# Kernel tuning notes

Measured on AMD Instinct MI355X. Metric: run time of the kernel, lower is better.

## Reference

```python
import jax, jax.numpy as jnp
import numpy as np

DIM = 4096
N_HEADS = 32
N_KV_HEADS = 8
HEAD_DIM = DIM // N_HEADS  # 128
B, S = 2, 2048
LN_EPS = 1e-5


def _precompute_freqs_cis(seqlen, head_dim, theta=10000.0):
    inv = 1.0 / (theta ** (np.arange(0, head_dim, 2, dtype=np.float32) / head_dim))  # [HD/2]
    ang = np.outer(np.arange(seqlen, dtype=np.float32), inv)  # [S, HD/2]
    return jnp.asarray(np.stack([np.cos(ang), np.sin(ang)], axis=-1))  # [S, HD/2, 2]


def setup_inputs() -> dict:
    key = jax.random.key(0)
    ks = jax.random.split(key, 9)
    std = 0.02
    return {
        "x": jax.random.normal(ks[0], (B, S, DIM), dtype=jnp.float32),
        "freqs_cis": _precompute_freqs_cis(S, HEAD_DIM),
        "wq": jax.random.normal(ks[1], (N_HEADS * HEAD_DIM, DIM), dtype=jnp.float32) * std,
        "wk": jax.random.normal(ks[2], (N_KV_HEADS * HEAD_DIM, DIM), dtype=jnp.float32) * std,
        "wv": jax.random.normal(ks[3], (N_KV_HEADS * HEAD_DIM, DIM), dtype=jnp.float32) * std,
        "wo": jax.random.normal(ks[4], (DIM, N_HEADS * HEAD_DIM), dtype=jnp.float32) * std,
        "q_norm_w": jnp.ones((N_HEADS * HEAD_DIM,), dtype=jnp.float32),
        "q_norm_b": jnp.zeros((N_HEADS * HEAD_DIM,), dtype=jnp.float32),
        "k_norm_w": jnp.ones((N_KV_HEADS * HEAD_DIM,), dtype=jnp.float32),
        "k_norm_b": jnp.zeros((N_KV_HEADS * HEAD_DIM,), dtype=jnp.float32),
    }


def _layernorm(v, w, b):
    mu = jnp.mean(v, axis=-1, keepdims=True)
    var = jnp.var(v, axis=-1, keepdims=True)
    return (v - mu) * jax.lax.rsqrt(var + LN_EPS) * w + b


def _rope(t, fc):
    # t: [B, S, nh, HD]; fc: [S, HD/2, 2] = (cos, sin)
    b_, s_, nh, hd = t.shape
    tr = t.reshape(b_, s_, nh, hd // 2, 2)
    a, bb = tr[..., 0], tr[..., 1]
    cos = fc[None, :, None, :, 0]
    sin = fc[None, :, None, :, 1]
    out = jnp.stack([a * cos - bb * sin, a * sin + bb * cos], axis=-1)
    return out.reshape(t.shape)


def reference(x, freqs_cis, wq, wk, wv, wo, q_norm_w, q_norm_b, k_norm_w, k_norm_b):
    bsz, seqlen, _ = x.shape
    H, KV, HD = N_HEADS, N_KV_HEADS, HEAD_DIM
    R = H // KV  # GQA repeat factor

    xq = jnp.einsum('bsd,ed->bse', x, wq)
    xk = jnp.einsum('bsd,ed->bse', x, wk)
    xv = jnp.einsum('bsd,ed->bse', x, wv)

    xq = _layernorm(xq, q_norm_w, q_norm_b)
    xk = _layernorm(xk, k_norm_w, k_norm_b)

    xq = xq.reshape(bsz, seqlen, H, HD)
    xk = xk.reshape(bsz, seqlen, KV, HD)
    xv = xv.reshape(bsz, seqlen, KV, HD)

    xq = _rope(xq, freqs_cis)
    xk = _rope(xk, freqs_cis)

    # GQA: group q heads as (kv, rep) and broadcast k/v instead of materializing repeats
    xqg = xq.reshape(bsz, seqlen, KV, R, HD)
    scale = 1.0 / jnp.sqrt(jnp.float32(HD))
    scores = jnp.einsum('bqkrh,bskh->bkrqs', xqg, xk) * scale  # [B,KV,R,S,S]
    attn = jax.nn.softmax(scores, axis=-1)
    out = jnp.einsum('bkrqs,bskh->bqkrh', attn, xv).reshape(bsz, seqlen, H * HD)
    return jnp.einsum('bse,de->bsd', out, wo)
```

## Files before the change

kernel.cpp:

```cpp
#include <hip/hip_runtime.h>
#include <cstdint>

typedef _Float16 half4v __attribute__((ext_vector_type(4)));
typedef _Float16 half8v __attribute__((ext_vector_type(8)));
typedef __fp16   fp16x2 __attribute__((ext_vector_type(2)));
typedef float    f32x4v __attribute__((ext_vector_type(4)));

#define DIM    4096
#define SEQ    2048
#define NBATCH 2
#define NHEAD  32
#define NKVH   8
#define HDIM   128
#define MROWS  (NBATCH*SEQ)
#define QKV_N  6144
#define KOFF   4096
#define VOFF   5120

__device__ __forceinline__ void gl_lds16(const _Float16* g, _Float16* l) {
  __builtin_amdgcn_global_load_lds(
      (const __attribute__((address_space(1))) void*)g,
      (__attribute__((address_space(3))) void*)l, 16, 0, 0);
}

__global__ __launch_bounds__(256) void cvt_kernel(const float* __restrict__ in,
                                                  _Float16* __restrict__ out, int n8) {
  int stride = gridDim.x * blockDim.x;
  for (int i = blockIdx.x * blockDim.x + threadIdx.x; i < n8; i += stride) {
    const float4* p = (const float4*)(in + (size_t)i * 8);
    float4 a = p[0], b = p[1];
    half8v h;
    h[0] = (_Float16)a.x; h[1] = (_Float16)a.y; h[2] = (_Float16)a.z; h[3] = (_Float16)a.w;
    h[4] = (_Float16)b.x; h[5] = (_Float16)b.y; h[6] = (_Float16)b.z; h[7] = (_Float16)b.w;
    *(half8v*)(out + (size_t)i * 8) = h;
  }
}

template<int OUTF16>
__global__ __launch_bounds__(256, 2) void gemm_bt(const _Float16* __restrict__ A,
                                                  const _Float16* __restrict__ B,
                                                  void* __restrict__ Cp, int N, int K) {
  __shared__ __align__(16) _Float16 As[128 * 64];
  __shared__ __align__(16) _Float16 Bs[128 * 64];
  const int tid = threadIdx.x, lane = tid & 63, w = tid >> 6;
  const int g = lane >> 4, li = lane & 15;
  const int bm = blockIdx.y * 128, bn = blockIdx.x * 128;
  const int wr = (w >> 1) * 64, wc = (w & 1) * 64;
  f32x4v acc[4][4] = {};
  const int srow = lane >> 3;
  const int scol = (lane & 7) * 8;
  const _Float16* Abase = A + (size_t)bm * K + scol;
  const _Float16* Bbase = B + (size_t)bn * K + scol;
  const int nkt = K >> 6;
  for (int kt = 0; kt < nkt; ++kt) {
#pragma unroll
    for (int i = 0; i < 4; ++i) {
      const int chunk = i * 4 + w;
      const int row = chunk * 8 + srow;
      gl_lds16(Abase + (size_t)row * K + kt * 64, As + chunk * 512);
      gl_lds16(Bbase + (size_t)row * K + kt * 64, Bs + chunk * 512);
    }
    __syncthreads();
#pragma unroll
    for (int kk = 0; kk < 2; ++kk) {
      half8v af[4], bf[4];
#pragma unroll
      for (int mi = 0; mi < 4; ++mi)
        af[mi] = *(const half8v*)(As + (wr + mi * 16 + li) * 64 + kk * 32 + g * 8);
#pragma unroll
      for (int ni = 0; ni < 4; ++ni)
        bf[ni] = *(const half8v*)(Bs + (wc + ni * 16 + li) * 64 + kk * 32 + g * 8);
#pragma unroll
      for (int mi = 0; mi < 4; ++mi)
#pragma unroll
        for (int ni = 0; ni < 4; ++ni)
          acc[mi][ni] = __builtin_amdgcn_mfma_f32_16x16x32_f16(af[mi], bf[ni], acc[mi][ni], 0, 0, 0);
    }
    __syncthreads();
  }
  const int r0 = bm + wr + g * 4, c0 = bn + wc + li;
#pragma unroll
  for (int mi = 0; mi < 4; ++mi)
#pragma unroll
    for (int ni = 0; ni < 4; ++ni)
#pragma unroll
      for (int j = 0; j < 4; ++j) {
        size_t idx = (size_t)(r0 + mi * 16 + j) * N + (c0 + ni * 16);
        if (OUTF16) ((_Float16*)Cp)[idx] = (_Float16)acc[mi][ni][j];
        else        ((float*)Cp)[idx]    = acc[mi][ni][j];
      }
}

template<int E>
__global__ __launch_bounds__(256) void ln_rope(_Float16* __restrict__ t, int ldt,
                                               const float* __restrict__ gw,
                                               const float* __restrict__ gb,
                                               const float* __restrict__ fc) {
  constexpr int EPT = E / 256;
  const int row = blockIdx.x;
  const int s = row & (SEQ - 1);
  const int tid = threadIdx.x, lane = tid & 63, w = tid >> 6;
  _Float16* rp = t + (size_t)row * ldt + tid * EPT;
  float v[EPT];
#pragma unroll
  for (int i = 0; i < EPT; i += 4) {
    half4v hv = *(const half4v*)(rp + i);
    v[i] = (float)hv[0]; v[i+1] = (float)hv[1]; v[i+2] = (float)hv[2]; v[i+3] = (float)hv[3];
  }
  float sum = 0.f, ssq = 0.f;
#pragma unroll
  for (int i = 0; i < EPT; ++i) { sum += v[i]; ssq += v[i] * v[i]; }
#pragma unroll
  for (int off = 1; off < 64; off <<= 1) { sum += __shfl_xor(sum, off); ssq += __shfl_xor(ssq, off); }
  __shared__ float red[8];
  if (lane == 0) { red[w] = sum; red[4 + w] = ssq; }
  __syncthreads();
  sum = red[0] + red[1] + red[2] + red[3];
  ssq = red[4] + red[5] + red[6] + red[7];
  const float mu = sum * (1.0f / E);
  const float rstd = rsqrtf(ssq * (1.0f / E) - mu * mu + 1e-5f);
  float ov[EPT];
#pragma unroll
  for (int i = 0; i < EPT; i += 2) {
    int e = tid * EPT + i;
    int hd = e & (HDIM - 1);
    float2 cs = *(const float2*)(fc + (size_t)s * HDIM + (hd >> 1) * 2);
    float a = (v[i]   - mu) * rstd * gw[e]   + gb[e];
    float b = (v[i+1] - mu) * rstd * gw[e+1] + gb[e+1];
    ov[i]   = a * cs.x - b * cs.y;
    ov[i+1] = a * cs.y + b * cs.x;
  }
#pragma unroll
  for (int i = 0; i < EPT; i += 4) {
    half4v hv;
    hv[0] = (_Float16)ov[i];   hv[1] = (_Float16)ov[i+1];
    hv[2] = (_Float16)ov[i+2]; hv[3] = (_Float16)ov[i+3];
    *(half4v*)(rp + i) = hv;
  }
}

__global__ __launch_bounds__(256, 2) void attn_kernel(const _Float16* __restrict__ QKV,
                                                      _Float16* __restrict__ Oa) {
  __shared__ __align__(16) _Float16 Ksh[2][64 * 128];
  __shared__ __align__(16) char Vt[128 * 128];
  const int tid = threadIdx.x, lane = tid & 63, w = tid >> 6;
  const int g = lane >> 4, li = lane & 15;
  const int blk = blockIdx.x;
  const int qt = blk & 31, h = (blk >> 5) & 31, b = blk >> 10;
  const int kvh = h >> 2;
  const size_t LD = QKV_N;
  const _Float16* Qb = QKV + (size_t)(b * SEQ) * LD + h * HDIM;
  const _Float16* Kb = QKV + (size_t)(b * SEQ) * LD + KOFF + kvh * HDIM;
  const _Float16* Vb = QKV + (size_t)(b * SEQ) * LD + VOFF + kvh * HDIM;
  const int qrow = qt * 64 + w * 16 + li;
  half8v qf[4];
#pragma unroll
  for (int kk = 0; kk < 4; ++kk) {
    half8v q0 = *(const half8v*)(Qb + (size_t)qrow * LD + kk * 32 + g * 8);
#pragma unroll
    for (int e = 0; e < 8; ++e) q0[e] = q0[e] * (_Float16)0.08838834764831845f;
    qf[kk] = q0;
  }
  float mrow = -1e30f, lrow = 0.f;
  f32x4v oacc[8] = {};
  uint4 va[2], vb2[2];
  const int lg = lane >> 4;
  const int gbit = (lane >> 5) & 1;
  const int ksc8 = ((lane & 15) ^ (((tid & 63) >> 4) & 7)) * 8;
  (void)ksc8;
#pragma unroll
  for (int i = 0; i < 4; ++i) {
    int chunk = i * 4 + w;
    int r = chunk * 4 + lg;
    int sc8 = ((lane & 15) ^ (r & 7)) * 8;
    gl_lds16(Kb + (size_t)r * LD + sc8, Ksh[0] + chunk * 512);
  }
#pragma unroll
  for (int i = 0; i < 2; ++i) {
    int p = tid + 256 * i; int v2 = p >> 4, c8 = p & 15;
    va[i]  = *(const uint4*)(Vb + (size_t)(v2 * 2)     * LD + c8 * 8);
    vb2[i] = *(const uint4*)(Vb + (size_t)(v2 * 2 + 1) * LD + c8 * 8);
  }
  const int NT = SEQ / 64;
  for (int kt = 0; kt < NT; ++kt) {
    __syncthreads();
#pragma unroll
    for (int i = 0; i < 2; ++i) {
      int p = tid + 256 * i; int v2 = p >> 4, c8 = p & 15;
      const uint32_t* a0 = (const uint32_t*)&va[i];
      const uint32_t* a1 = (const uint32_t*)&vb2[i];
      int slot = v2 >> 2, bofs = (v2 & 3) << 2;
#pragma unroll
      for (int wi = 0; wi < 4; ++wi) {
        uint32_t ev = __builtin_amdgcn_perm(a1[wi], a0[wi], 0x05040100u);
        uint32_t od = __builtin_amdgcn_perm(a1[wi], a0[wi], 0x07060302u);
        int hd0 = c8 * 8 + 2 * wi, hd1 = hd0 + 1;
        int k0 = ((hd0 >> 3) ^ hd0) & 7, k1 = ((hd1 >> 3) ^ hd1) & 7;
        *(uint32_t*)(Vt + hd0 * 128 + ((slot ^ k0) << 4) + bofs) = ev;
        *(uint32_t*)(Vt + hd1 * 128 + ((slot ^ k1) << 4) + bofs) = od;
      }
    }
    __syncthreads();
    if (kt + 1 < NT) {
#pragma unroll
      for (int i = 0; i < 2; ++i) {
        int p = tid + 256 * i; int v2 = p >> 4, c8 = p & 15;
        va[i]  = *(const uint4*)(Vb + (size_t)((kt + 1) * 64 + v2 * 2)     * LD + c8 * 8);
        vb2[i] = *(const uint4*)(Vb + (size_t)((kt + 1) * 64 + v2 * 2 + 1) * LD + c8 * 8);
      }
    }
    const _Float16* Kcur = Ksh[kt & 1];
    f32x4v sc[4] = {};
    __builtin_amdgcn_s_setprio(1);
#pragma unroll
    for (int kk = 0; kk < 4; ++kk) {
#pragma unroll
      for (int ni = 0; ni < 4; ++ni) {
        half8v kf = *(const half8v*)(Kcur + (16 * ni + li) * 128 + ((4 * kk + g) ^ (li & 7)) * 8);
        sc[ni] = __builtin_amdgcn_mfma_f32_16x16x32_f16(kf, qf[kk], sc[ni], 0, 0, 0);
      }
    }
    __builtin_amdgcn_s_setprio(0);
    if (kt + 1 < NT) {
      _Float16* Knxt = Ksh[(kt + 1) & 1];
#pragma unroll
      for (int i = 0; i < 4; ++i) {
        int chunk = i * 4 + w;
        int r = chunk * 4 + lg;
        int sc8 = ((lane & 15) ^ (r & 7)) * 8;
        gl_lds16(Kb + (size_t)((kt + 1) * 64 + r) * LD + sc8, Knxt + chunk * 512);
      }
    }
    float m16 = sc[0][0];
#pragma unroll
    for (int ni = 0; ni < 4; ++ni) {
      m16 = fmaxf(m16, fmaxf(fmaxf(sc[ni][0], sc[ni][1]), fmaxf(sc[ni][2], sc[ni][3])));
    }
    m16 = fmaxf(m16, __shfl_xor(m16, 16));
    m16 = fmaxf(m16, __shfl_xor(m16, 32));
    if (!__all(m16 - mrow <= 8.0f)) {
      const float mn = fmaxf(mrow, m16);
      const float sfo = __expf(mrow - mn);
      mrow = mn;
      lrow *= sfo;
      float sfj[4];
#pragma unroll
      for (int j = 0; j < 4; ++j) sfj[j] = __shfl(sfo, (lane & 48) | (4 * g + j));
#pragma unroll
      for (int nio = 0; nio < 8; ++nio) {
        oacc[nio][0] *= sfj[0]; oacc[nio][1] *= sfj[1];
        oacc[nio][2] *= sfj[2]; oacc[nio][3] *= sfj[3];
      }
    }
    float pp[4][4];
    float rs = 0.f;
#pragma unroll
    for (int ni = 0; ni < 4; ++ni)
#pragma unroll
      for (int j = 0; j < 4; ++j) { float pv = __expf(sc[ni][j] - mrow); pp[ni][j] = pv; rs += pv; }
    rs += __shfl_xor(rs, 16); rs += __shfl_xor(rs, 32);
    lrow += rs;
    uint32_t u[4][2];
#pragma unroll
    for (int ni = 0; ni < 4; ++ni) {
      fp16x2 p0 = __builtin_amdgcn_cvt_pkrtz(pp[ni][0], pp[ni][1]);
      fp16x2 p1 = __builtin_amdgcn_cvt_pkrtz(pp[ni][2], pp[ni][3]);
      u[ni][0] = *(uint32_t*)&p0;
      u[ni][1] = *(uint32_t*)&p1;
    }
#pragma unroll
    for (int kk = 0; kk < 2; ++kk) {
      uint32_t own0 = gbit ? u[2*kk+1][0] : u[2*kk][0];
      uint32_t own1 = gbit ? u[2*kk+1][1] : u[2*kk][1];
      uint32_t oth0 = gbit ? u[2*kk][0]   : u[2*kk+1][0];
      uint32_t oth1 = gbit ? u[2*kk][1]   : u[2*kk+1][1];
      uint32_t r16_0 = (uint32_t)__shfl_xor((int)own0, 16);
      uint32_t r16_1 = (uint32_t)__shfl_xor((int)own1, 16);
      uint32_t r32_0 = (uint32_t)__shfl_xor((int)oth0, 32);
      uint32_t r32_1 = (uint32_t)__shfl_xor((int)oth1, 32);
      uint32_t r48_0 = (uint32_t)__shfl_xor((int)oth0, 48);
      uint32_t r48_1 = (uint32_t)__shfl_xor((int)oth1, 48);
      uint32_t d0 = (g == 0) ? own0 : (g == 1) ? r48_0 : (g == 2) ? r32_0 : r16_0;
      uint32_t d1 = (g == 0) ? own1 : (g == 1) ? r48_1 : (g == 2) ? r32_1 : r16_1;
      uint32_t d2 = (g == 0) ? r16_0 : (g == 1) ? r32_0 : (g == 2) ? r48_0 : own0;
      uint32_t d3 = (g == 0) ? r16_1 : (g == 1) ? r32_1 : (g == 2) ? r48_1 : own1;
      union { uint32_t u4[4]; half8v h; } pa;
      pa.u4[0] = d0; pa.u4[1] = d1; pa.u4[2] = d2; pa.u4[3] = d3;
      __builtin_amdgcn_s_setprio(1);
#pragma unroll
      for (int nio = 0; nio < 8; ++nio) {
        int r = nio * 16 + li;
        int key = ((r >> 3) ^ r) & 7;
        half8v bv = *(const half8v*)(Vt + r * 128 + (((kk * 4 + g) ^ key) << 4));
        oacc[nio] = __builtin_amdgcn_mfma_f32_16x16x32_f16(pa.h, bv, oacc[nio], 0, 0, 0);
      }
      __builtin_amdgcn_s_setprio(0);
    }
  }
  float rinv[4];
#pragma unroll
  for (int j = 0; j < 4; ++j)
    rinv[j] = 1.0f / __shfl(lrow, (lane & 48) | (4 * g + j));
  _Float16* Ob = Oa + (size_t)(b * SEQ + qt * 64 + w * 16) * DIM + h * HDIM;
#pragma unroll
  for (int j = 0; j < 4; ++j)
#pragma unroll
    for (int nio = 0; nio < 8; ++nio)
      Ob[(size_t)(4 * g + j) * DIM + nio * 16 + li] = (_Float16)(oacc[nio][j] * rinv[j]);
}

extern "C" void kernel_launch(void* const* d_in, const int* in_sizes, int n_in,
                              void* d_out, int out_size, void* d_ws, size_t ws_size,
                              hipStream_t stream) {
  const float* x   = (const float*)d_in[0];
  const float* fc  = (const float*)d_in[1];
  const float* wq  = (const float*)d_in[2];
  const float* wk  = (const float*)d_in[3];
  const float* wv  = (const float*)d_in[4];
  const float* wo  = (const float*)d_in[5];
  const float* qnw = (const float*)d_in[6];
  const float* qnb = (const float*)d_in[7];
  const float* knw = (const float*)d_in[8];
  const float* knb = (const float*)d_in[9];
  float* out = (float*)d_out;
  (void)in_sizes; (void)n_in; (void)out_size;

  const size_t MB = 1024 * 1024;
  if (ws_size < 128 * MB) return;
  char* ws = (char*)d_ws;
  _Float16* x_h    = (_Float16*)(ws + 0);
  _Float16* wqkv_h = (_Float16*)(ws + 32 * MB);
  _Float16* wk_h   = (_Float16*)(ws + 64 * MB);
  _Float16* wv_h   = (_Float16*)(ws + 72 * MB);
  _Float16* qkv_h  = (_Float16*)(ws + 80 * MB);
  _Float16* wo_h   = wqkv_h;
  _Float16* ao_h   = x_h;

  cvt_kernel<<<2048, 256, 0, stream>>>(x,  x_h,    (MROWS * DIM) / 8);
  cvt_kernel<<<2048, 256, 0, stream>>>(wq, wqkv_h, (DIM * DIM) / 8);
  cvt_kernel<<<1024, 256, 0, stream>>>(wk, wk_h,   (1024 * DIM) / 8);
  cvt_kernel<<<1024, 256, 0, stream>>>(wv, wv_h,   (1024 * DIM) / 8);

  gemm_bt<1><<<dim3(QKV_N / 128, MROWS / 128), 256, 0, stream>>>(x_h, wqkv_h, qkv_h, QKV_N, DIM);

  cvt_kernel<<<2048, 256, 0, stream>>>(wo, wo_h, (DIM * DIM) / 8);

  ln_rope<4096><<<MROWS, 256, 0, stream>>>(qkv_h,        QKV_N, qnw, qnb, fc);
  ln_rope<1024><<<MROWS, 256, 0, stream>>>(qkv_h + KOFF, QKV_N, knw, knb, fc);

  attn_kernel<<<NBATCH * NHEAD * (SEQ / 64), 256, 0, stream>>>(qkv_h, ao_h);

  gemm_bt<0><<<dim3(DIM / 128, MROWS / 128), 256, 0, stream>>>(ao_h, wo_h, out, DIM, DIM);
}
```

Before: 751.1 us.

## Replace GEMM with 256x256 double-buffered ping-pong pipelined MFMA kernel

Replaces the 128x128 single-buffered GEMM with a 256x256-tile, 512-thread kernel. It double-buffers A and B in LDS with staggered half-tile prefetches, uses XOR-swizzled LDS layouts, and sets s_setprio around the MFMA quarters. A remapped workgroup order groups neighbouring tiles for better L2 reuse. The aim is to hide global-load latency and cut LDS bank conflicts in both projection GEMMs, at the cost of 128KB of LDS per block, lower occupancy, and fragile hand-placed waitcnt and barrier ordering.

```diff
diff --git a/kernel.cpp b/kernel.cpp
--- a/kernel.cpp
+++ b/kernel.cpp
@@ -36,51 +36,126 @@
   }
 }
 
+
+#define SBAR() do { asm volatile("" ::: "memory"); \
+                    __builtin_amdgcn_s_barrier();  \
+                    asm volatile("" ::: "memory"); } while (0)
+#define LGK0() asm volatile("s_waitcnt lgkmcnt(0)" ::: "memory")
+#define VM6()  asm volatile("s_waitcnt vmcnt(6)" ::: "memory")
+#define VM0()  asm volatile("s_waitcnt vmcnt(0)" ::: "memory")
+
+#define STAGE_HALF(Gm, rowbase, kidx, h, buf) do {                                   \
+    gl_lds16((Gm) + (size_t)((rowbase) + (h)*128 + srow) * K + (kidx)*64 + sslot8,   \
+             (buf) + (h)*8192 + w*512);                                              \
+    gl_lds16((Gm) + (size_t)((rowbase) + (h)*128 + 64 + srow) * K + (kidx)*64 + sslot8, \
+             (buf) + (h)*8192 + 4096 + w*512);                                       \
+  } while (0)
+
+#define MFMA_Q(hm, hn, bf)                                                   \
+    _Pragma("unroll") for (int kk = 0; kk < 2; ++kk)                         \
+      _Pragma("unroll") for (int mi = 0; mi < 4; ++mi)                       \
+        _Pragma("unroll") for (int ni = 0; ni < 2; ++ni)                     \
+          acc[(hm) * 4 + mi][(hn) * 2 + ni] =                                \
+              __builtin_amdgcn_mfma_f32_16x16x32_f16(                        \
+                  a[mi][kk], bf[ni][kk], acc[(hm) * 4 + mi][(hn) * 2 + ni], 0, 0, 0)
+
+#define KSTEP(kcur, AC, BC, AN)                                              \
+  do {                                                                       \
+    const int k_ = (kcur);                                                   \
+    half8v a[4][2], b0[2][2], b1[2][2];                                      \
+                                         \
+    _Pragma("unroll") for (int mi = 0; mi < 4; ++mi)                         \
+      _Pragma("unroll") for (int kk = 0; kk < 2; ++kk)                       \
+        a[mi][kk] = *(const half8v*)((AC) + (wm * 128 + mi * 16 + li) * 64 + \
+                                     (((kk * 4 + g) ^ li7) * 8));            \
+    _Pragma("unroll") for (int ni = 0; ni < 2; ++ni)                         \
+      _Pragma("unroll") for (int kk = 0; kk < 2; ++kk)                       \
+        b0[ni][kk] = *(const half8v*)((BC) + (wn * 64 + ni * 16 + li) * 64 + \
+                                      (((kk * 4 + g) ^ li7) * 8));           \
+    if (k_ + 1 < nkt) STAGE_HALF(A, bm, k_ + 1, 1, (AN));                    \
+    SBAR(); LGK0();                                                          \
+    __builtin_amdgcn_s_setprio(1);                                           \
+    MFMA_Q(0, 0, b0);                                                        \
+    __builtin_amdgcn_s_setprio(0);                                           \
+    SBAR();                                                                  \
+                                         \
+    _Pragma("unroll") for (int ni = 0; ni < 2; ++ni)                         \
+      _Pragma("unroll") for (int kk = 0; kk < 2; ++kk)                       \
+        b1[ni][kk] = *(const half8v*)((BC) + (wn * 64 + 32 + ni * 16 + li) * 64 + \
+                                      (((kk * 4 + g) ^ li7) * 8));           \
+    SBAR(); LGK0();                                                          \
+    __builtin_amdgcn_s_setprio(1);                                           \
+    MFMA_Q(0, 1, b1);                                                        \
+    __builtin_amdgcn_s_setprio(0);                                           \
+    SBAR();                                                                  \
+          \
+    _Pragma("unroll") for (int mi = 0; mi < 4; ++mi)                         \
+      _Pragma("unroll") for (int kk = 0; kk < 2; ++kk)                       \
+        a[mi][kk] = *(const half8v*)((AC) + (wm * 128 + 64 + mi * 16 + li) * 64 + \
+                                     (((kk * 4 + g) ^ li7) * 8));            \
+    if (k_ + 2 < nkt) {                                                      \
+      STAGE_HALF(B, bn, k_ + 2, 0, (BC));                                    \
+      STAGE_HALF(B, bn, k_ + 2, 1, (BC));                                    \
+    }                                                                        \
+    SBAR(); LGK0();                                                          \
+    __builtin_amdgcn_s_setprio(1);                                           \
+    MFMA_Q(1, 1, b1);                                                        \
+    __builtin_amdgcn_s_setprio(0);                                           \
+    SBAR();                                                                  \
+          \
+    if (k_ + 2 < nkt) STAGE_HALF(A, bm, k_ + 2, 0, (AC));                    \
+    SBAR();                                                                  \
+    __builtin_amdgcn_s_setprio(1);                                           \
+    MFMA_Q(1, 0, b0);                                                        \
+    __builtin_amdgcn_s_setprio(0);                                           \
+    if (k_ + 2 < nkt) { VM6(); } else if (k_ + 1 < nkt) { VM0(); }           \
+    SBAR();                                                                  \
+  } while (0)
+
 template<int OUTF16>
-__global__ __launch_bounds__(256, 2) void gemm_bt(const _Float16* __restrict__ A,
+__global__ __launch_bounds__(512, 2) void gemm256(const _Float16* __restrict__ A,
                                                   const _Float16* __restrict__ B,
-                                                  void* __restrict__ Cp, int N, int K) {
-  __shared__ __align__(16) _Float16 As[128 * 64];
-  __shared__ __align__(16) _Float16 Bs[128 * 64];
+                                                  void* __restrict__ Cp,
+                                                  int N, int K, int nbx) {
+  __shared__ __align__(16) _Float16 As[2][256 * 64];
+  __shared__ __align__(16) _Float16 Bs[2][256 * 64];
   const int tid = threadIdx.x, lane = tid & 63, w = tid >> 6;
-  const int g = lane >> 4, li = lane & 15;
-  const int bm = blockIdx.y * 128, bn = blockIdx.x * 128;
-  const int wr = (w >> 1) * 64, wc = (w & 1) * 64;
-  f32x4v acc[4][4] = {};
-  const int srow = lane >> 3;
-  const int scol = (lane & 7) * 8;
-  const _Float16* Abase = A + (size_t)bm * K + scol;
-  const _Float16* Bbase = B + (size_t)bn * K + scol;
+  const int g = lane >> 4, li = lane & 15, li7 = lane & 7;
+  const int wm = w >> 2, wn = w & 3;
+  const int nwg = gridDim.x, orig = blockIdx.x;
+  const int wgid = (nwg & 7) ? orig : ((orig & 7) * (nwg >> 3) + (orig >> 3));
+  const int bm = (wgid / nbx) * 256, bn = (wgid % nbx) * 256;
+  const int srow = tid >> 3;
+  const int sslot8 = ((lane & 7) ^ ((lane >> 3) & 7)) * 8;
   const int nkt = K >> 6;
-  for (int kt = 0; kt < nkt; ++kt) {
-#pragma unroll
-    for (int i = 0; i < 4; ++i) {
-      const int chunk = i * 4 + w;
-      const int row = chunk * 8 + srow;
-      gl_lds16(Abase + (size_t)row * K + kt * 64, As + chunk * 512);
-      gl_lds16(Bbase + (size_t)row * K + kt * 64, Bs + chunk * 512);
-    }
-    __syncthreads();
-#pragma unroll
-    for (int kk = 0; kk < 2; ++kk) {
-      half8v af[4], bf[4];
-#pragma unroll
-      for (int mi = 0; mi < 4; ++mi)
-        af[mi] = *(const half8v*)(As + (wr + mi * 16 + li) * 64 + kk * 32 + g * 8);
-#pragma unroll
-      for (int ni = 0; ni < 4; ++ni)
-        bf[ni] = *(const half8v*)(Bs + (wc + ni * 16 + li) * 64 + kk * 32 + g * 8);
-#pragma unroll
-      for (int mi = 0; mi < 4; ++mi)
-#pragma unroll
-        for (int ni = 0; ni < 4; ++ni)
-          acc[mi][ni] = __builtin_amdgcn_mfma_f32_16x16x32_f16(af[mi], bf[ni], acc[mi][ni], 0, 0, 0);
-    }
-    __syncthreads();
-  }
-  const int r0 = bm + wr + g * 4, c0 = bn + wc + li;
-#pragma unroll
-  for (int mi = 0; mi < 4; ++mi)
+  _Float16* As0 = &As[0][0]; _Float16* As1 = &As[1][0];
+  _Float16* Bs0 = &Bs[0][0]; _Float16* Bs1 = &Bs[1][0];
+
+  f32x4v acc[8][4] = {};
+
+  STAGE_HALF(A, bm, 0, 0, As0);
+  STAGE_HALF(A, bm, 0, 1, As0);
+  STAGE_HALF(B, bn, 0, 0, Bs0);
+  STAGE_HALF(B, bn, 0, 1, Bs0);
+  if (nkt > 1) {
+    STAGE_HALF(B, bn, 1, 0, Bs1);
+    STAGE_HALF(B, bn, 1, 1, Bs1);
+    STAGE_HALF(A, bm, 1, 0, As1);
+    VM6();
+  } else {
+    VM0();
+  }
+  SBAR();
+
+  for (int k = 0; k < nkt; k += 2) {
+    KSTEP(k,     As0, Bs0, As1);
+    KSTEP(k + 1, As1, Bs1, As0);
+  }
+
+  const int r0 = bm + wm * 128 + g * 4;
+  const int c0 = bn + wn * 64 + li;
+#pragma unroll
+  for (int mi = 0; mi < 8; ++mi)
 #pragma unroll
     for (int ni = 0; ni < 4; ++ni)
 #pragma unroll
@@ -166,8 +241,6 @@
   uint4 va[2], vb2[2];
   const int lg = lane >> 4;
   const int gbit = (lane >> 5) & 1;
-  const int ksc8 = ((lane & 15) ^ (((tid & 63) >> 4) & 7)) * 8;
-  (void)ksc8;
 #pragma unroll
   for (int i = 0; i < 4; ++i) {
     int chunk = i * 4 + w;
@@ -341,7 +414,8 @@
   cvt_kernel<<<1024, 256, 0, stream>>>(wk, wk_h,   (1024 * DIM) / 8);
   cvt_kernel<<<1024, 256, 0, stream>>>(wv, wv_h,   (1024 * DIM) / 8);
 
-  gemm_bt<1><<<dim3(QKV_N / 128, MROWS / 128), 256, 0, stream>>>(x_h, wqkv_h, qkv_h, QKV_N, DIM);
+  gemm256<1><<<(MROWS / 256) * (QKV_N / 256), 512, 0, stream>>>(x_h, wqkv_h, qkv_h,
+                                                                QKV_N, DIM, QKV_N / 256);
 
   cvt_kernel<<<2048, 256, 0, stream>>>(wo, wo_h, (DIM * DIM) / 8);
 
@@ -350,5 +424,6 @@
 
   attn_kernel<<<NBATCH * NHEAD * (SEQ / 64), 256, 0, stream>>>(qkv_h, ao_h);
 
-  gemm_bt<0><<<dim3(DIM / 128, MROWS / 128), 256, 0, stream>>>(ao_h, wo_h, out, DIM, DIM);
-}
+  gemm256<0><<<(MROWS / 256) * (DIM / 256), 512, 0, stream>>>(ao_h, wo_h, out,
+                                                              DIM, DIM, DIM / 256);
+}
```

Measured after the change: 689.0 us. -8.3%, faster.
